# Kernel tuning notes

Measured on AMD Instinct MI355X. Metric: run time of the kernel, lower is better.

## Reference

```python
import jax, jax.numpy as jnp
import numpy as np

B, L, H, I, N, R, K = 2, 1024, 2048, 4096, 16, 128, 4


def setup_inputs() -> dict:
    key = jax.random.key(0)
    ks = jax.random.split(key, 8)
    sc = lambda k, shape, s: jax.random.normal(k, shape, dtype=jnp.float32) * s
    x = jax.random.normal(ks[0], (B, L, H), dtype=jnp.float32)
    in_proj_w = sc(ks[1], (2 * I, H), 0.02)
    conv_w = sc(ks[2], (I, 1, K), 0.2)
    conv_b = jnp.zeros((I,), jnp.float32)
    x_proj_w = sc(ks[3], (R + 2 * N, I), 0.02)
    dt_proj_w = sc(ks[4], (I, R), 0.05)
    dt_proj_b = sc(ks[5], (I,), 0.5) - 2.0  # dt bias init skews small dt after softplus
    A_log = jnp.log(jnp.broadcast_to(jnp.arange(1, N + 1, dtype=jnp.float32)[None, :], (I, N)))
    D = jnp.ones((I,), jnp.float32)
    out_proj_w = sc(ks[6], (H, I), 0.02)
    return dict(x=x, in_proj_w=in_proj_w, conv_w=conv_w, conv_b=conv_b,
                x_proj_w=x_proj_w, dt_proj_w=dt_proj_w, dt_proj_b=dt_proj_b,
                A_log=A_log, D=D, out_proj_w=out_proj_w)


def reference(x, in_proj_w, conv_w, conv_b, x_proj_w, dt_proj_w, dt_proj_b, A_log, D, out_proj_w):
    # x: [B,L,H]
    nI, nK = conv_w.shape[0], conv_w.shape[2]
    nR = dt_proj_w.shape[1]
    nN = A_log.shape[1]
    proj = jnp.einsum('blh,ph->blp', x, in_proj_w)           # [B,L,2I]
    h_in, gate = jnp.split(proj, 2, axis=-1)                 # [B,L,I] each
    # causal depthwise conv1d (torch pads K-1 both sides then slices [:L] == left-pad K-1)
    hc = jnp.transpose(h_in, (0, 2, 1))                      # [B,I,L]
    hc = jax.lax.conv_general_dilated(hc, conv_w, (1,), [(nK - 1, 0)],
                                      dimension_numbers=('NCH', 'OIH', 'NCH'),
                                      feature_group_count=nI)
    u = jax.nn.silu(hc + conv_b[None, :, None])              # [B,I,L]
    uT = jnp.transpose(u, (0, 2, 1))                         # [B,L,I]
    ssm = jnp.einsum('bli,pi->blp', uT, x_proj_w)            # [B,L,R+2N]
    ts, Bm, Cm = jnp.split(ssm, [nR, nR + nN], axis=-1)
    dt = jax.nn.softplus(jnp.einsum('blr,ir->bli', ts, dt_proj_w) + dt_proj_b)  # [B,L,I]
    A = -jnp.exp(A_log)                                      # [I,N]
    dA = jnp.exp(dt[..., None] * A[None, None])              # [B,L,I,N]
    dBx = (dt * uT)[..., None] * Bm[:, :, None, :]           # [B,L,I,N]

    def combine(c1, c2):
        a1, b1 = c1
        a2, b2 = c2
        return a2 * a1, a2 * b1 + b2

    _, hstates = jax.lax.associative_scan(combine, (dA, dBx), axis=1)  # [B,L,I,N]
    y = jnp.einsum('blin,bln->bli', hstates, Cm) + D * uT    # [B,L,I]
    y = y * jax.nn.silu(gate)
    return jnp.einsum('bli,hi->blh', y, out_proj_w)          # [B,L,H]
```

## Files before the change

### kernel.cpp

```cpp
#include <hip/hip_runtime.h>
#include <math.h>

constexpr int Bc = 2, Lc = 1024, Hc = 2048, Ic = 4096, Nc = 16, Rc = 128;
constexpr int Mrows = Bc * Lc;
constexpr int Pc = Rc + 2 * Nc;
constexpr int TWOI = 2 * Ic;
constexpr int NCH = 16;
constexpr int CL = Lc / NCH;
constexpr int KS = 8;
constexpr int KCH = Ic / KS;

typedef __attribute__((ext_vector_type(8))) short s16x8;
typedef __attribute__((ext_vector_type(8))) unsigned short u16x8;
typedef __attribute__((ext_vector_type(4))) float f32x4;

__device__ __forceinline__ unsigned short f2bf(float f) {
  union { float f; unsigned int u; } v; v.f = f;
  unsigned int r = v.u + 0x7fffu + ((v.u >> 16) & 1u);
  return (unsigned short)(r >> 16);
}
__device__ __forceinline__ float bf2f(unsigned short u) {
  union { unsigned int u; float f; } v; v.u = ((unsigned int)u) << 16;
  return v.f;
}

__device__ __forceinline__ void gload16(const void* g, void* l) {
  __builtin_amdgcn_global_load_lds(
      (const __attribute__((address_space(1))) unsigned int*)g,
      (__attribute__((address_space(3))) unsigned int*)l, 16, 0, 0);
}

__global__ __launch_bounds__(256) void cvt_f32_bf16(const float* __restrict__ in,
                                                    unsigned short* __restrict__ out,
                                                    size_t n8) {
  size_t t = (size_t)blockIdx.x * 256 + threadIdx.x;
  if (t >= n8) return;
  size_t i = t * 8;
  float4 a = *reinterpret_cast<const float4*>(in + i);
  float4 b = *reinterpret_cast<const float4*>(in + i + 4);
  u16x8 o;
  o[0] = f2bf(a.x); o[1] = f2bf(a.y); o[2] = f2bf(a.z); o[3] = f2bf(a.w);
  o[4] = f2bf(b.x); o[5] = f2bf(b.y); o[6] = f2bf(b.z); o[7] = f2bf(b.w);
  *reinterpret_cast<u16x8*>(out + i) = o;
}

__global__ __launch_bounds__(512, 2) void gemm256_bf16_nt(
    const unsigned short* __restrict__ A, int lda,
    const unsigned short* __restrict__ W, int ldw,
    unsigned short* __restrict__ C, int ldc, int Kdim) {
  __shared__ unsigned short lds[2 * 32768];
  const int tid = threadIdx.x;
  const int lane = tid & 63;
  const int wave = tid >> 6;
  const int wr = wave >> 2;
  const int wc = wave & 3;
  const int r15 = lane & 15;
  const int kg = lane >> 4;

  int gx = gridDim.x;
  int lin = blockIdx.y * gx + blockIdx.x;
  int cpx = (gx * gridDim.y) >> 3;
  int nlin = (lin & 7) * cpx + (lin >> 3);
  const int bm = (nlin / gx) * 256;
  const int bn = (nlin % gx) * 256;

  const int s0 = tid,       j0 = s0 ^ ((s0 >> 3) & 7);
  const int s1 = 512 + tid, j1 = s1 ^ ((s1 >> 3) & 7);
  const int ar0 = j0 >> 3, ac0 = (j0 & 7) * 8;
  const int ar1 = j1 >> 3, ac1 = (j1 & 7) * 8;

  f32x4 acc[8][4];
#pragma unroll
  for (int mf = 0; mf < 8; mf++)
#pragma unroll
    for (int nf = 0; nf < 4; nf++) acc[mf][nf] = (f32x4){0.f, 0.f, 0.f, 0.f};

  const unsigned short* Abase = A + (size_t)bm * lda;
  const unsigned short* Wbase = W + (size_t)bn * ldw;

  auto stage = [&](int kt, int d) {
    const unsigned short* Ab = Abase + kt * 64;
    const unsigned short* Wb = Wbase + kt * 64;
    unsigned short* l = lds + d * 32768;
    gload16(Ab + (size_t)ar0 * lda + ac0,         l + s0 * 8);
    gload16(Ab + (size_t)ar1 * lda + ac1,         l + s1 * 8);
    gload16(Ab + (size_t)(128 + ar0) * lda + ac0, l + 8192 + s0 * 8);
    gload16(Ab + (size_t)(128 + ar1) * lda + ac1, l + 8192 + s1 * 8);
    gload16(Wb + (size_t)ar0 * ldw + ac0,         l + 16384 + s0 * 8);
    gload16(Wb + (size_t)ar1 * ldw + ac1,         l + 16384 + s1 * 8);
    gload16(Wb + (size_t)(128 + ar0) * ldw + ac0, l + 24576 + s0 * 8);
    gload16(Wb + (size_t)(128 + ar1) * ldw + ac1, l + 24576 + s1 * 8);
  };

  const int abase = wr * 8192;
  const int bbase = 16384 + (wc >> 1) * 8192;
  const int brow0 = (wc & 1) * 64;
  const int sw7 = r15 & 7;

  const int NT = Kdim >> 6;
  stage(0, 0);
  __syncthreads();

  for (int t = 0; t < NT; t++) {
    const int d = t & 1;
    if (t + 1 < NT) stage(t + 1, d ^ 1);
    const unsigned short* lb = lds + d * 32768;
    s16x8 afr[4], bfr[4];
#pragma unroll
    for (int kk = 0; kk < 2; kk++) {
      const int swzk = ((kk * 4 + kg) ^ sw7) * 8;
#pragma unroll
      for (int nf = 0; nf < 4; nf++) {
        int rb = brow0 + nf * 16 + r15;
        bfr[nf] = *reinterpret_cast<const s16x8*>(lb + bbase + rb * 64 + swzk);
      }
#pragma unroll
      for (int mf = 0; mf < 4; mf++) {
        int ra = mf * 16 + r15;
        afr[mf] = *reinterpret_cast<const s16x8*>(lb + abase + ra * 64 + swzk);
      }
      __builtin_amdgcn_s_setprio(1);
#pragma unroll
      for (int mf = 0; mf < 4; mf++)
#pragma unroll
        for (int nf = 0; nf < 4; nf++)
          acc[mf][nf] = __builtin_amdgcn_mfma_f32_16x16x32_bf16(afr[mf], bfr[nf], acc[mf][nf], 0, 0, 0);
      __builtin_amdgcn_s_setprio(0);
#pragma unroll
      for (int mf = 0; mf < 4; mf++) {
        int ra = (mf + 4) * 16 + r15;
        afr[mf] = *reinterpret_cast<const s16x8*>(lb + abase + ra * 64 + swzk);
      }
      __builtin_amdgcn_s_setprio(1);
#pragma unroll
      for (int mf = 0; mf < 4; mf++)
#pragma unroll
        for (int nf = 0; nf < 4; nf++)
          acc[mf + 4][nf] = __builtin_amdgcn_mfma_f32_16x16x32_bf16(afr[mf], bfr[nf], acc[mf + 4][nf], 0, 0, 0);
      __builtin_amdgcn_s_setprio(0);
    }
    __syncthreads();
  }

  const int cm0 = bm + wr * 128 + kg * 4;
  const int cn0 = bn + wc * 64 + r15;
#pragma unroll
  for (int mf = 0; mf < 8; mf++)
#pragma unroll
    for (int nf = 0; nf < 4; nf++)
#pragma unroll
      for (int r = 0; r < 4; r++)
        C[(size_t)(cm0 + mf * 16 + r) * ldc + cn0 + nf * 16] = f2bf(acc[mf][nf][r]);
}

template <int EPI, int OBF>
__global__ __launch_bounds__(256) void gemm_bf16_nt(const unsigned short* __restrict__ A, int lda,
                                                    const unsigned short* __restrict__ W, int ldw,
                                                    void* __restrict__ Cv, int ldc, int Kdim,
                                                    const float* __restrict__ bias) {
  __shared__ unsigned short As[128 * 32];
  __shared__ unsigned short Bs[128 * 32];
  const int tid = threadIdx.x;
  const int lane = tid & 63;
  const int wave = tid >> 6;
  const int wr = wave >> 1, wc = wave & 1;
  const int bm = blockIdx.y * 128, bn = blockIdx.x * 128;

  f32x4 acc[4][4];
#pragma unroll
  for (int mt = 0; mt < 4; mt++)
#pragma unroll
    for (int nt = 0; nt < 4; nt++) acc[mt][nt] = (f32x4){0.f, 0.f, 0.f, 0.f};

  const int srow = tid >> 2;
  const int scol = (tid & 3) * 8;
  const unsigned short* Ag = A + (size_t)(bm + srow) * lda + scol;
  const unsigned short* Wg = W + (size_t)(bn + srow) * ldw + scol;
  unsigned short* Al = As + tid * 8;
  unsigned short* Wl = Bs + tid * 8;

  const unsigned short* aRd = As + (wr * 64 + (lane & 15)) * 32 + (lane >> 4) * 8;
  const unsigned short* bRd = Bs + (wc * 64 + (lane & 15)) * 32 + (lane >> 4) * 8;

  for (int k0 = 0; k0 < Kdim; k0 += 32) {
    __syncthreads();
    gload16(Ag + k0, Al);
    gload16(Ag + k0 + (size_t)64 * lda, Al + 64 * 32);
    gload16(Wg + k0, Wl);
    gload16(Wg + k0 + (size_t)64 * ldw, Wl + 64 * 32);
    __syncthreads();
    s16x8 af[4], bw[4];
#pragma unroll
    for (int mt = 0; mt < 4; mt++) af[mt] = *reinterpret_cast<const s16x8*>(aRd + mt * 16 * 32);
#pragma unroll
    for (int nt = 0; nt < 4; nt++) bw[nt] = *reinterpret_cast<const s16x8*>(bRd + nt * 16 * 32);
#pragma unroll
    for (int mt = 0; mt < 4; mt++)
#pragma unroll
      for (int nt = 0; nt < 4; nt++)
        acc[mt][nt] = __builtin_amdgcn_mfma_f32_16x16x32_bf16(af[mt], bw[nt], acc[mt][nt], 0, 0, 0);
  }

  const int cm0 = bm + wr * 64 + (lane >> 4) * 4;
  const int cn0 = bn + wc * 64 + (lane & 15);
#pragma unroll
  for (int mt = 0; mt < 4; mt++)
#pragma unroll
    for (int nt = 0; nt < 4; nt++)
#pragma unroll
      for (int r = 0; r < 4; r++) {
        float c = acc[mt][nt][r];
        int n = cn0 + nt * 16;
        if (EPI == 1) {
          float xx = c + bias[n];
          c = (xx > 20.f) ? xx : log1pf(__expf(xx));
        }
        size_t idx = (size_t)(cm0 + mt * 16 + r) * ldc + n;
        if (OBF)
          ((unsigned short*)Cv)[idx] = f2bf(c);
        else
          ((float*)Cv)[idx] = c;
      }
}

__global__ __launch_bounds__(256) void ssm_bf16_kernel(const unsigned short* __restrict__ ub,
                                                       const unsigned short* __restrict__ wb,
                                                       float* __restrict__ part) {
  const int tid = threadIdx.x;
  const int lane = tid & 63;
  const int wave = tid >> 6;
  const int mt = blockIdx.x;
  const int ks = blockIdx.y;
  const int r15 = lane & 15;
  const int kg = (lane >> 4) * 8;

  const unsigned short* Arow = ub + (size_t)(mt * 64 + wave * 16 + r15) * Ic + ks * KCH + kg;
  const unsigned short* Brow = wb + (size_t)r15 * Ic + ks * KCH + kg;

  f32x4 acc[10];
#pragma unroll
  for (int nt = 0; nt < 10; nt++) acc[nt] = (f32x4){0.f, 0.f, 0.f, 0.f};

#pragma unroll 2
  for (int kk = 0; kk < KCH; kk += 32) {
    s16x8 af = *reinterpret_cast<const s16x8*>(Arow + kk);
#pragma unroll
    for (int nt = 0; nt < 10; nt++) {
      s16x8 bf = *reinterpret_cast<const s16x8*>(Brow + (size_t)nt * 16 * Ic + kk);
      acc[nt] = __builtin_amdgcn_mfma_f32_16x16x32_bf16(af, bf, acc[nt], 0, 0, 0);
    }
  }

  const int m0 = mt * 64 + wave * 16 + (lane >> 4) * 4;
  float* po = part + ((size_t)ks * Mrows + m0) * Pc;
#pragma unroll
  for (int nt = 0; nt < 10; nt++)
#pragma unroll
    for (int r = 0; r < 4; r++)
      po[(size_t)r * Pc + nt * 16 + r15] = acc[nt][r];
}

__global__ __launch_bounds__(256) void ssm_reduce(const float* __restrict__ part,
                                                  float* __restrict__ ssm,
                                                  unsigned short* __restrict__ tsb) {
  int t = blockIdx.x * 256 + threadIdx.x;
  float s = 0.f;
#pragma unroll
  for (int ks = 0; ks < KS; ks++) s += part[(size_t)ks * Mrows * Pc + t];
  ssm[t] = s;
  int m = t / Pc, n = t - m * Pc;
  if (n < Rc) tsb[(size_t)m * Rc + n] = f2bf(s);
}

__global__ __launch_bounds__(256) void conv_silu_kernel(const unsigned short* __restrict__ projb,
                                                        const float* __restrict__ cw,
                                                        const float* __restrict__ cb,
                                                        unsigned short* __restrict__ ub) {
  int t = blockIdx.x * 256 + threadIdx.x;
  int i = t & (Ic - 1);
  int m = t >> 12;
  int l = m & (Lc - 1);
  float4 w4 = *reinterpret_cast<const float4*>(&cw[i * 4]);
  float wk[4] = {w4.x, w4.y, w4.z, w4.w};
  float acc = cb[i];
#pragma unroll
  for (int k = 0; k < 4; k++) {
    int ll = l - 3 + k;
    if (ll >= 0) acc = fmaf(wk[k], bf2f(projb[(size_t)(m - 3 + k) * TWOI + i]), acc);
  }
  float s = acc / (1.f + __expf(-acc));
  ub[(size_t)m * Ic + i] = f2bf(s);
}

__global__ __launch_bounds__(256) void scan_pass1(const float* __restrict__ dt,
                                                  const unsigned short* __restrict__ ub,
                                                  const float* __restrict__ ssm,
                                                  const float* __restrict__ A_log,
                                                  float* __restrict__ sc1) {
  constexpr int IB = Ic / 256;
  int ib = blockIdx.x % IB;
  int c = (blockIdx.x / IB) % NCH;
  int b = blockIdx.x / (IB * NCH);
  int i = ib * 256 + threadIdx.x;

  float Ac[Nc];
#pragma unroll
  for (int n = 0; n < Nc; n++) Ac[n] = -__expf(A_log[i * Nc + n]);
  float Ap[Nc], h[Nc];
#pragma unroll
  for (int n = 0; n < Nc; n++) { Ap[n] = 1.f; h[n] = 0.f; }

  int l0 = c * CL;
  for (int l = l0; l < l0 + CL; l++) {
    int m = b * Lc + l;
    float dtv = dt[(size_t)m * Ic + i];
    float uv = bf2f(ub[(size_t)m * Ic + i]);
    float du = dtv * uv;
#pragma unroll
    for (int n = 0; n < Nc; n++) {
      float Bv = ssm[m * Pc + Rc + n];
      float dA = __expf(dtv * Ac[n]);
      h[n] = fmaf(dA, h[n], du * Bv);
      Ap[n] *= dA;
    }
  }
  size_t off = ((size_t)(b * Ic + i) * NCH + c) * 32;
#pragma unroll
  for (int n = 0; n < Nc; n++) {
    sc1[off + n] = Ap[n];
    sc1[off + 16 + n] = h[n];
  }
}

__global__ __launch_bounds__(256) void scan_mid(const float* __restrict__ sc1,
                                                float* __restrict__ sc2) {
  int t = blockIdx.x * 256 + threadIdx.x;
  int n = t & 15;
  int bi = t >> 4;
  float h = 0.f;
  size_t base = (size_t)bi * NCH;
  for (int c = 0; c < NCH; c++) {
    sc2[(base + c) * 16 + n] = h;
    float Ap = sc1[(base + c) * 32 + n];
    float he = sc1[(base + c) * 32 + 16 + n];
    h = fmaf(Ap, h, he);
  }
}

__global__ __launch_bounds__(256) void scan_pass3(const float* __restrict__ dt,
                                                  const unsigned short* __restrict__ ub,
                                                  const float* __restrict__ ssm,
                                                  const float* __restrict__ A_log,
                                                  const float* __restrict__ Dp,
                                                  const float* __restrict__ sc2,
                                                  const unsigned short* __restrict__ projb,
                                                  unsigned short* __restrict__ yb) {
  constexpr int IB = Ic / 256;
  int ib = blockIdx.x % IB;
  int c = (blockIdx.x / IB) % NCH;
  int b = blockIdx.x / (IB * NCH);
  int i = ib * 256 + threadIdx.x;

  float Ac[Nc];
#pragma unroll
  for (int n = 0; n < Nc; n++) Ac[n] = -__expf(A_log[i * Nc + n]);
  float h[Nc];
  size_t hoff = ((size_t)(b * Ic + i) * NCH + c) * 16;
#pragma unroll
  for (int n = 0; n < Nc; n++) h[n] = sc2[hoff + n];
  float Dv = Dp[i];

  int l0 = c * CL;
  for (int l = l0; l < l0 + CL; l++) {
    int m = b * Lc + l;
    float dtv = dt[(size_t)m * Ic + i];
    float uv = bf2f(ub[(size_t)m * Ic + i]);
    float du = dtv * uv;
    float acc = Dv * uv;
#pragma unroll
    for (int n = 0; n < Nc; n++) {
      float Bv = ssm[m * Pc + Rc + n];
      float Cv = ssm[m * Pc + Rc + Nc + n];
      float dA = __expf(dtv * Ac[n]);
      h[n] = fmaf(dA, h[n], du * Bv);
      acc = fmaf(h[n], Cv, acc);
    }
    float g = bf2f(projb[(size_t)m * TWOI + Ic + i]);
    float sg = g / (1.f + __expf(-g));
    yb[(size_t)m * Ic + i] = f2bf(acc * sg);
  }
}

extern "C" void kernel_launch(void* const* d_in, const int* in_sizes, int n_in,
                              void* d_out, int out_size, void* d_ws, size_t ws_size,
                              hipStream_t stream) {
  const float* x = (const float*)d_in[0];
  const float* in_proj_w = (const float*)d_in[1];
  const float* conv_w = (const float*)d_in[2];
  const float* conv_b = (const float*)d_in[3];
  const float* x_proj_w = (const float*)d_in[4];
  const float* dt_proj_w = (const float*)d_in[5];
  const float* dt_proj_b = (const float*)d_in[6];
  const float* A_log = (const float*)d_in[7];
  const float* Dp = (const float*)d_in[8];
  const float* out_proj_w = (const float*)d_in[9];
  float* out = (float*)d_out;

  char* base = (char*)d_ws;
  unsigned short* projb = (unsigned short*)base; base += (size_t)Mrows * TWOI * 2;
  unsigned short* ub = (unsigned short*)base;    base += (size_t)Mrows * Ic * 2;
  float* ssm = (float*)base;                     base += (size_t)Mrows * Pc * 4;
  unsigned short* tsb = (unsigned short*)base;   base += (size_t)Mrows * Rc * 2;
  char* dtb = base;                              base += (size_t)Mrows * Ic * 4;
  float* dt = (float*)dtb;
  float* part = (float*)dtb;
  unsigned short* owb = (unsigned short*)dtb;
  char* xbb = base;                              base += (size_t)Mrows * Hc * 2;
  unsigned short* xb = (unsigned short*)xbb;
  unsigned short* wb160 = (unsigned short*)xbb;
  unsigned short* dtwb = (unsigned short*)(xbb + 2 * 1024 * 1024);
  char* wbase = base;                            base += (size_t)TWOI * Hc * 2;
  unsigned short* wb = (unsigned short*)wbase;
  float* sc1 = (float*)wbase;
  unsigned short* yb = (unsigned short*)wbase;
  float* sc2 = (float*)(wbase + (size_t)Bc * Ic * NCH * 32 * 4);
  size_t need = (size_t)(base - (char*)d_ws);
  if (ws_size < need) return;

  dim3 blk(256);

  cvt_f32_bf16<<<(Mrows * (size_t)Hc / 8 + 255) / 256, blk, 0, stream>>>(x, xb, Mrows * (size_t)Hc / 8);
  cvt_f32_bf16<<<((size_t)TWOI * Hc / 8 + 255) / 256, blk, 0, stream>>>(in_proj_w, wb, (size_t)TWOI * Hc / 8);

  gemm256_bf16_nt<<<dim3(TWOI / 256, Mrows / 256), dim3(512), 0, stream>>>(
      xb, Hc, wb, Hc, projb, TWOI, Hc);

  cvt_f32_bf16<<<((size_t)Pc * Ic / 8 + 255) / 256, blk, 0, stream>>>(x_proj_w, wb160, (size_t)Pc * Ic / 8);
  cvt_f32_bf16<<<((size_t)Ic * Rc / 8 + 255) / 256, blk, 0, stream>>>(dt_proj_w, dtwb, (size_t)Ic * Rc / 8);

  conv_silu_kernel<<<(size_t)Mrows * Ic / 256, blk, 0, stream>>>(projb, conv_w, conv_b, ub);

  ssm_bf16_kernel<<<dim3(Mrows / 64, KS), blk, 0, stream>>>(ub, wb160, part);
  ssm_reduce<<<Mrows * Pc / 256, blk, 0, stream>>>(part, ssm, tsb);

  gemm_bf16_nt<1, 0><<<dim3(Ic / 128, Mrows / 128), blk, 0, stream>>>(
      tsb, Rc, dtwb, Rc, dt, Ic, Rc, dt_proj_b);

  scan_pass1<<<Bc * NCH * (Ic / 256), blk, 0, stream>>>(dt, ub, ssm, A_log, sc1);
  scan_mid<<<Bc * Ic * Nc / 256, blk, 0, stream>>>(sc1, sc2);
  scan_pass3<<<Bc * NCH * (Ic / 256), blk, 0, stream>>>(dt, ub, ssm, A_log, Dp, sc2, projb, yb);

  cvt_f32_bf16<<<((size_t)Hc * Ic / 8 + 255) / 256, blk, 0, stream>>>(out_proj_w, owb, (size_t)Hc * Ic / 8);

  gemm_bf16_nt<0, 0><<<dim3(Hc / 128, Mrows / 128), blk, 0, stream>>>(
      yb, Ic, owb, Ic, out, Hc, Ic, nullptr);
}
```

Before: 375.6 us.

## Run out_proj GEMM as split-K on the 256-tile kernel with a reduce pass

The final out projection (M=2048, N=2048, K=4096) moves from the 128x128-tile GEMM onto the 256x256-tile MFMA kernel, with K split four ways across blockIdx.z. Each split writes an fp32 partial into reused workspace buffers, and a separate kernel then sums the four partials into the output. The aim is to fill the GPU with enough blocks while using the larger tile's better data reuse. In exchange it adds 4x fp32 partial-write traffic, an extra reduce launch, and relies on the aliased workspace regions being free at that point.

```diff
diff --git a/kernel.cpp b/kernel.cpp
--- a/kernel.cpp
+++ b/kernel.cpp
@@ -44,10 +44,11 @@
   *reinterpret_cast<u16x8*>(out + i) = o;
 }
 
+template <int OBF>
 __global__ __launch_bounds__(512, 2) void gemm256_bf16_nt(
     const unsigned short* __restrict__ A, int lda,
     const unsigned short* __restrict__ W, int ldw,
-    unsigned short* __restrict__ C, int ldc, int Kdim) {
+    void* C0, void* C1, void* C2, void* C3, int ldc, int Kdim) {
   __shared__ unsigned short lds[2 * 32768];
   const int tid = threadIdx.x;
   const int lane = tid & 63;
@@ -57,6 +58,10 @@
   const int r15 = lane & 15;
   const int kg = lane >> 4;
 
+  const int ks = blockIdx.z;
+  void* Cv = (ks == 0) ? C0 : (ks == 1) ? C1 : (ks == 2) ? C2 : C3;
+  const int koff = ks * Kdim;
+
   int gx = gridDim.x;
   int lin = blockIdx.y * gx + blockIdx.x;
   int cpx = (gx * gridDim.y) >> 3;
@@ -75,8 +80,8 @@
 #pragma unroll
     for (int nf = 0; nf < 4; nf++) acc[mf][nf] = (f32x4){0.f, 0.f, 0.f, 0.f};
 
-  const unsigned short* Abase = A + (size_t)bm * lda;
-  const unsigned short* Wbase = W + (size_t)bn * ldw;
+  const unsigned short* Abase = A + (size_t)bm * lda + koff;
+  const unsigned short* Wbase = W + (size_t)bn * ldw + koff;
 
   auto stage = [&](int kt, int d) {
     const unsigned short* Ab = Abase + kt * 64;
@@ -149,8 +154,31 @@
 #pragma unroll
     for (int nf = 0; nf < 4; nf++)
 #pragma unroll
-      for (int r = 0; r < 4; r++)
-        C[(size_t)(cm0 + mf * 16 + r) * ldc + cn0 + nf * 16] = f2bf(acc[mf][nf][r]);
+      for (int r = 0; r < 4; r++) {
+        size_t idx = (size_t)(cm0 + mf * 16 + r) * ldc + cn0 + nf * 16;
+        if (OBF)
+          ((unsigned short*)Cv)[idx] = f2bf(acc[mf][nf][r]);
+        else
+          ((float*)Cv)[idx] = acc[mf][nf][r];
+      }
+}
+
+__global__ __launch_bounds__(256) void out_reduce(const float* __restrict__ p0,
+                                                  const float* __restrict__ p1,
+                                                  const float* __restrict__ p2,
+                                                  const float* __restrict__ p3,
+                                                  float* __restrict__ out) {
+  size_t t = ((size_t)blockIdx.x * 256 + threadIdx.x) * 4;
+  float4 a = *reinterpret_cast<const float4*>(p0 + t);
+  float4 b = *reinterpret_cast<const float4*>(p1 + t);
+  float4 c = *reinterpret_cast<const float4*>(p2 + t);
+  float4 d = *reinterpret_cast<const float4*>(p3 + t);
+  float4 r;
+  r.x = a.x + b.x + c.x + d.x;
+  r.y = a.y + b.y + c.y + d.y;
+  r.z = a.z + b.z + c.z + d.z;
+  r.w = a.w + b.w + c.w + d.w;
+  *reinterpret_cast<float4*>(out + t) = r;
 }
 
 template <int EPI, int OBF>
@@ -427,13 +455,19 @@
   size_t need = (size_t)(base - (char*)d_ws);
   if (ws_size < need) return;
 
+  const size_t Q = (size_t)Mrows * Hc * 4;
+  float* op0 = (float*)((char*)projb);
+  float* op1 = (float*)((char*)projb + Q);
+  float* op2 = (float*)((char*)ub);
+  float* op3 = (float*)(dtb + Q);
+
   dim3 blk(256);
 
   cvt_f32_bf16<<<(Mrows * (size_t)Hc / 8 + 255) / 256, blk, 0, stream>>>(x, xb, Mrows * (size_t)Hc / 8);
   cvt_f32_bf16<<<((size_t)TWOI * Hc / 8 + 255) / 256, blk, 0, stream>>>(in_proj_w, wb, (size_t)TWOI * Hc / 8);
 
-  gemm256_bf16_nt<<<dim3(TWOI / 256, Mrows / 256), dim3(512), 0, stream>>>(
-      xb, Hc, wb, Hc, projb, TWOI, Hc);
+  gemm256_bf16_nt<1><<<dim3(TWOI / 256, Mrows / 256, 1), dim3(512), 0, stream>>>(
+      xb, Hc, wb, Hc, projb, projb, projb, projb, TWOI, Hc);
 
   cvt_f32_bf16<<<((size_t)Pc * Ic / 8 + 255) / 256, blk, 0, stream>>>(x_proj_w, wb160, (size_t)Pc * Ic / 8);
   cvt_f32_bf16<<<((size_t)Ic * Rc / 8 + 255) / 256, blk, 0, stream>>>(dt_proj_w, dtwb, (size_t)Ic * Rc / 8);
@@ -452,6 +486,7 @@
 
   cvt_f32_bf16<<<((size_t)Hc * Ic / 8 + 255) / 256, blk, 0, stream>>>(out_proj_w, owb, (size_t)Hc * Ic / 8);
 
-  gemm_bf16_nt<0, 0><<<dim3(Hc / 128, Mrows / 128), blk, 0, stream>>>(
-      yb, Ic, owb, Ic, out, Hc, Ic, nullptr);
-}
+  gemm256_bf16_nt<0><<<dim3(Hc / 256, Mrows / 256, 4), dim3(512), 0, stream>>>(
+      yb, Ic, owb, Ic, op0, op1, op2, op3, Hc, Ic / 4);
+  out_reduce<<<(Mrows * (size_t)Hc / 4) / 256, blk, 0, stream>>>(op0, op1, op2, op3, out);
+}
```

New measurement: 340.4 us. 9.4% less time.
